# Kernel tuning notes

Measured on AMD Instinct MI355X. Metric: run time of the kernel, lower is better.

## Reference

```python
import jax, jax.numpy as jnp
import numpy as np

N = 50000      # nodes
E = 100000     # edges
F_NODE = 128
F_EDGE = 16
H = 64         # hidden_dim
OUT = 32
STEPS = 3
G = 64         # num_graphs (static; batch.max()+1 in torch)


def setup_inputs() -> dict:
    key = jax.random.key(0)
    ks = jax.random.split(key, 20)

    def lin(k, fin, fout):
        s = 1.0 / np.sqrt(fin)
        return jax.random.uniform(k, (fin, fout), jnp.float32, -s, s)

    def bias(k, fin, fout):
        s = 1.0 / np.sqrt(fin)
        return jax.random.uniform(k, (fout,), jnp.float32, -s, s)

    inp = {
        'x': jax.random.normal(ks[0], (N, F_NODE), jnp.float32),
        'edge_index': jax.random.randint(ks[1], (2, E), 0, N),
        'edge_attr': jax.random.normal(ks[2], (E, F_EDGE), jnp.float32),
        'batch': jnp.sort(jax.random.randint(ks[3], (N,), 0, G)),
        # node encoder
        'W_enc': lin(ks[4], F_NODE, H), 'b_enc': bias(ks[5], F_NODE, H),
        # edge_nn: Linear(F_EDGE,H) -> ReLU -> Linear(H, H*H)
        'W_e1': lin(ks[6], F_EDGE, H), 'b_e1': bias(ks[7], F_EDGE, H),
        'W_e2': lin(ks[8], H, H * H), 'b_e2': bias(ks[9], H, H * H),
        # GRUCell (torch layout: [3H, H])
        'W_ih': jax.random.uniform(ks[10], (3 * H, H), jnp.float32, -1/np.sqrt(H), 1/np.sqrt(H)),
        'W_hh': jax.random.uniform(ks[11], (3 * H, H), jnp.float32, -1/np.sqrt(H), 1/np.sqrt(H)),
        'b_ih': jax.random.uniform(ks[12], (3 * H,), jnp.float32, -1/np.sqrt(H), 1/np.sqrt(H)),
        'b_hh': jax.random.uniform(ks[13], (3 * H,), jnp.float32, -1/np.sqrt(H), 1/np.sqrt(H)),
        # readout MLP: Linear(H,H) -> ReLU -> Linear(H,OUT)
        'W_r1': lin(ks[14], H, H), 'b_r1': bias(ks[15], H, H),
        'W_r2': lin(ks[16], H, OUT), 'b_r2': bias(ks[17], H, OUT),
    }
    return inp


def gru_cell(m, h, W_ih, W_hh, b_ih, b_hh):
    gi = m @ W_ih.T + b_ih   # [N, 3H]
    gh = h @ W_hh.T + b_hh
    i_r, i_z, i_n = jnp.split(gi, 3, axis=-1)
    h_r, h_z, h_n = jnp.split(gh, 3, axis=-1)
    r = jax.nn.sigmoid(i_r + h_r)
    z = jax.nn.sigmoid(i_z + h_z)
    n = jnp.tanh(i_n + r * h_n)
    return (1.0 - z) * n + z * h


def reference(x, edge_index, edge_attr, batch, W_enc, b_enc, W_e1, b_e1,
              W_e2, b_e2, W_ih, W_hh, b_ih, b_hh, W_r1, b_r1, W_r2, b_r2):
    h = x @ W_enc + b_enc                                   # [N, H]
    src, dst = edge_index[0], edge_index[1]
    # edge-conditioned weight matrices (loop-invariant; compute once)
    ew = (jax.nn.relu(edge_attr @ W_e1 + b_e1) @ W_e2 + b_e2).reshape(E, H, H)
    for _ in range(STEPS):
        msg = jnp.einsum('eij,ej->ei', ew, h[src])          # per-edge matvec
        m_agg = jax.ops.segment_sum(msg, dst, num_segments=N)
        h = gru_cell(m_agg, h, W_ih, W_hh, b_ih, b_hh)
    g = jax.ops.segment_sum(h, batch, num_segments=G)       # sum readout
    return jax.nn.relu(g @ W_r1 + b_r1) @ W_r2 + b_r2
```

## Files before the change

kernel.cpp:

```cpp
#include <hip/hip_runtime.h>
#include <hip/hip_bf16.h>
#include <math.h>

#define NN 50000
#define NE 100000
#define FN 128
#define FE 16
#define HD 64
#define OUTD 32
#define NG 64
#define ZK 65

typedef unsigned int uint;
typedef unsigned short ushort;
typedef __attribute__((ext_vector_type(8))) short short8;
typedef __attribute__((ext_vector_type(16))) float f32x16;

static __device__ __forceinline__ float bfbits2f(uint u) {
    return __builtin_bit_cast(float, u << 16);
}
static __device__ __forceinline__ uint packbf(float f0, float f1) {
    return __builtin_amdgcn_perm(__builtin_bit_cast(uint, f1),
                                 __builtin_bit_cast(uint, f0), 0x07060302u);
}
static __device__ __forceinline__ ushort f2bf(float f) {
    uint u = __builtin_bit_cast(uint, f);
    u = (u + 0x7FFFu + ((u >> 16) & 1u)) >> 16;
    return (ushort)u;
}
static __device__ __forceinline__ uint pack2rne(float f0, float f1) {
    return (uint)f2bf(f0) | ((uint)f2bf(f1) << 16);
}
static __device__ __forceinline__ float fsigmoid(float x) {
    return 1.f / (1.f + __expf(-x));
}
static __device__ __forceinline__ float ftanh(float x) {
    float t = __expf(2.f * x);
    return 1.f - 2.f / (t + 1.f);
}

#define PREP_S0 (ZK * 4096)
#define PREP_S1 (256 * 128)
__global__ void k_prep(const float* __restrict__ W_e2, const float* __restrict__ b_e2,
                       const float* __restrict__ W_ih, const float* __restrict__ W_hh,
                       ushort* __restrict__ Wtb, ushort* __restrict__ Bg) {
    int idx = blockIdx.x * 256 + threadIdx.x;
    if (idx < PREP_S0) {
        int k0 = idx >> 12, r = idx & 4095;
        int i = r >> 6, j = r & 63;
        float v = (k0 < 64) ? W_e2[k0 * 4096 + i * 64 + j] : b_e2[i * 64 + j];
        Wtb[idx] = f2bf(v);
        return;
    }
    idx -= PREP_S0;
    if (idx < PREP_S1) {
        int n = idx >> 7, k = idx & 127;
        int g = n >> 6, i = n & 63;
        float v = 0.f;
        if (g == 0)      v = (k < 64) ? W_ih[i * 64 + k]         : W_hh[i * 64 + (k - 64)];
        else if (g == 1) v = (k < 64) ? W_ih[(64 + i) * 64 + k]  : W_hh[(64 + i) * 64 + (k - 64)];
        else if (g == 2) v = (k < 64) ? W_ih[(128 + i) * 64 + k] : 0.f;
        else             v = (k < 64) ? 0.f                      : W_hh[(128 + i) * 64 + (k - 64)];
        Bg[idx] = f2bf(v);
    }
}

#define NBENC ((NN + 127) / 128)
#define NBEDG ((NE + 255) / 256)
__global__ __launch_bounds__(256, 2)
void k_enc_edge(const float* __restrict__ x, const float* __restrict__ W_enc,
                const float* __restrict__ b_enc,
                const float* __restrict__ ea, const float* __restrict__ W_e1,
                const float* __restrict__ b_e1,
                float* __restrict__ h, ushort* __restrict__ hb,
                ushort* __restrict__ zbT) {
    int t = threadIdx.x;
    if (blockIdx.x < NBENC) {
        __shared__ __align__(16) ushort blds[64 * 128];
        int wave = t >> 6, lane = t & 63, l31 = lane & 31, lhi = lane >> 5;
        for (int idx = t; idx < 1024; idx += 256) {
            int n = idx >> 4, p = idx & 15;
            int ssrc = p ^ (n & 15);
            int kk = ssrc * 8;
            uint4 u;
            u.x = pack2rne(W_enc[(kk + 0) * 64 + n], W_enc[(kk + 1) * 64 + n]);
            u.y = pack2rne(W_enc[(kk + 2) * 64 + n], W_enc[(kk + 3) * 64 + n]);
            u.z = pack2rne(W_enc[(kk + 4) * 64 + n], W_enc[(kk + 5) * 64 + n]);
            u.w = pack2rne(W_enc[(kk + 6) * 64 + n], W_enc[(kk + 7) * 64 + n]);
            *(uint4*)&blds[idx * 8] = u;
        }
        int node0 = blockIdx.x * 128 + wave * 32;
        int m = node0 + l31;
        int mc = (m < NN) ? m : NN - 1;
        short8 afr[8];
        const float* xr = x + (size_t)mc * 128;
        #pragma unroll
        for (int ks = 0; ks < 8; ks++) {
            float4 v0 = *(const float4*)(xr + ks * 16 + lhi * 8);
            float4 v1 = *(const float4*)(xr + ks * 16 + lhi * 8 + 4);
            uint4 u;
            u.x = pack2rne(v0.x, v0.y); u.y = pack2rne(v0.z, v0.w);
            u.z = pack2rne(v1.x, v1.y); u.w = pack2rne(v1.z, v1.w);
            afr[ks] = __builtin_bit_cast(short8, u);
        }
        __syncthreads();
        #pragma unroll
        for (int ct = 0; ct < 2; ct++) {
            f32x16 acc = {0};
            int n = ct * 32 + l31;
            #pragma unroll
            for (int ks = 0; ks < 8; ks++) {
                int sp = (ks * 2 + lhi) ^ (n & 15);
                short8 bf = *(const short8*)&blds[n * 128 + sp * 8];
                acc = __builtin_amdgcn_mfma_f32_32x32x16_bf16(afr[ks], bf, acc, 0, 0, 0);
            }
            int o = ct * 32 + l31;
            float bias = b_enc[o];
            #pragma unroll
            for (int r = 0; r < 16; r++) {
                int row = (r & 3) + 8 * (r >> 2) + 4 * lhi;
                int node = node0 + row;
                if (node < NN) {
                    float v = acc[r] + bias;
                    h[node * 64 + o] = v;
                    hb[node * 64 + o] = f2bf(v);
                }
            }
        }
    } else {
        __shared__ float Ws[16 * 64];
        __shared__ float b1s[64];
        for (int idx = t; idx < 1024; idx += 256) Ws[idx] = W_e1[idx];
        if (t < 64) b1s[t] = b_e1[t];
        __syncthreads();
        int e = (blockIdx.x - NBENC) * 256 + t;
        int ec = (e < NE) ? e : NE - 1;
        float eav[16];
        const float4* ep = (const float4*)(ea + ec * 16);
        #pragma unroll
        for (int q = 0; q < 4; q++) {
            float4 v = ep[q];
            eav[q * 4 + 0] = v.x; eav[q * 4 + 1] = v.y; eav[q * 4 + 2] = v.z; eav[q * 4 + 3] = v.w;
        }
        if (e >= NE) return;
        #pragma unroll 4
        for (int k = 0; k < 64; k++) {
            float acc = b1s[k];
            #pragma unroll
            for (int f = 0; f < 16; f++) acc += eav[f] * Ws[f * 64 + k];
            zbT[(size_t)k * NE + e] = f2bf(fmaxf(acc, 0.f));
        }
        zbT[(size_t)64 * NE + e] = f2bf(1.0f);
    }
}

__global__ __launch_bounds__(256, 2)
void k_message(const ushort* __restrict__ zbT, const ushort* __restrict__ hb,
               const int* __restrict__ eidx, const ushort* __restrict__ Wtb,
               float* __restrict__ m_agg) {
    __shared__ __align__(16) ushort wlds[2][2 * 4096];
    __shared__ __align__(16) ushort zlds[72 * 256];
    __shared__ int sdst[256];

    int t = threadIdx.x;
    int wave = t >> 6, lane = t & 63;
    int l31 = lane & 31, lhi = lane >> 5;
    int eblk = blockIdx.x * 256;
    int e0 = eblk + wave * 64;

    {
        int e = eblk + t; if (e >= NE) e = NE - 1;
        sdst[t] = eidx[NE + e];
    }

    float hf[2][32];
    #pragma unroll
    for (int mt = 0; mt < 2; mt++) {
        int e = e0 + mt * 32 + l31;
        int ec = (e < NE) ? e : NE - 1;
        int s = eidx[ec];
        const ushort* hrow = hb + (size_t)s * 64;
        #pragma unroll
        for (int c = 0; c < 4; c++) {
            uint4 v = *(const uint4*)(hrow + c * 16 + lhi * 8);
            hf[mt][c * 8 + 0] = bfbits2f(v.x & 0xFFFFu); hf[mt][c * 8 + 1] = bfbits2f(v.x >> 16);
            hf[mt][c * 8 + 2] = bfbits2f(v.y & 0xFFFFu); hf[mt][c * 8 + 3] = bfbits2f(v.y >> 16);
            hf[mt][c * 8 + 4] = bfbits2f(v.z & 0xFFFFu); hf[mt][c * 8 + 5] = bfbits2f(v.z >> 16);
            hf[mt][c * 8 + 6] = bfbits2f(v.w & 0xFFFFu); hf[mt][c * 8 + 7] = bfbits2f(v.w >> 16);
        }
    }

    #pragma unroll
    for (int call = 0; call < 9; call++) {
        int slot = call * 256 + t;
        int k0 = slot >> 5; if (k0 > 64) k0 = 64;
        int p = slot & 31;
        const ushort* src = zbT + (size_t)k0 * NE + eblk + p * 8;
        __builtin_amdgcn_global_load_lds(
            (const __attribute__((address_space(1))) void*)src,
            (__attribute__((address_space(3))) void*)&zlds[(size_t)(call * 256 + wave * 64) * 8],
            16, 0, 0);
    }

    auto stagew = [&](int slab0, int buf) {
        #pragma unroll
        for (int call = 0; call < 4; call++) {
            int slot = call * 256 + t;
            int slab = slab0 + (slot >> 9);
            if (slab > 64) slab = 64;
            int w = slot & 511;
            int i = w >> 3, jbp = w & 7;
            int jbg = jbp ^ (i & 7);
            const ushort* src = Wtb + (size_t)slab * 4096 + i * 64 + jbg * 8;
            __builtin_amdgcn_global_load_lds(
                (const __attribute__((address_space(1))) void*)src,
                (__attribute__((address_space(3))) void*)&wlds[buf][(size_t)(call * 256 + wave * 64) * 8],
                16, 0, 0);
        }
    };
    stagew(0, 0);

    f32x16 acc00 = {0}, acc01 = {0}, acc10 = {0}, acc11 = {0};

    for (int rnd = 0; rnd < 33; rnd++) {
        __syncthreads();
        int buf = rnd & 1;
        if (rnd < 32) stagew(2 * rnd + 2, buf ^ 1);
        int nk = (rnd < 32) ? 2 : 1;
        #pragma unroll 2
        for (int kk = 0; kk < nk; kk++) {
            int k0 = 2 * rnd + kk;
            float zf0 = bfbits2f((uint)zlds[k0 * 256 + wave * 64 + l31]);
            float zf1 = bfbits2f((uint)zlds[k0 * 256 + wave * 64 + 32 + l31]);
            const ushort* wb = &wlds[buf][kk * 4096];
            #pragma unroll
            for (int c = 0; c < 4; c++) {
                int jb = c * 2 + lhi;
                short8 b0 = *(const short8*)&wb[((0 * 32 + l31) << 6) + ((jb ^ (l31 & 7)) << 3)];
                short8 b1 = *(const short8*)&wb[((32 + l31) << 6) + ((jb ^ (l31 & 7)) << 3)];
                uint4 au0, au1;
                au0.x = packbf(zf0 * hf[0][c * 8 + 0], zf0 * hf[0][c * 8 + 1]);
                au0.y = packbf(zf0 * hf[0][c * 8 + 2], zf0 * hf[0][c * 8 + 3]);
                au0.z = packbf(zf0 * hf[0][c * 8 + 4], zf0 * hf[0][c * 8 + 5]);
                au0.w = packbf(zf0 * hf[0][c * 8 + 6], zf0 * hf[0][c * 8 + 7]);
                au1.x = packbf(zf1 * hf[1][c * 8 + 0], zf1 * hf[1][c * 8 + 1]);
                au1.y = packbf(zf1 * hf[1][c * 8 + 2], zf1 * hf[1][c * 8 + 3]);
                au1.z = packbf(zf1 * hf[1][c * 8 + 4], zf1 * hf[1][c * 8 + 5]);
                au1.w = packbf(zf1 * hf[1][c * 8 + 6], zf1 * hf[1][c * 8 + 7]);
                short8 a0 = __builtin_bit_cast(short8, au0);
                short8 a1 = __builtin_bit_cast(short8, au1);
                acc00 = __builtin_amdgcn_mfma_f32_32x32x16_bf16(a0, b0, acc00, 0, 0, 0);
                acc01 = __builtin_amdgcn_mfma_f32_32x32x16_bf16(a0, b1, acc01, 0, 0, 0);
                acc10 = __builtin_amdgcn_mfma_f32_32x32x16_bf16(a1, b0, acc10, 0, 0, 0);
                acc11 = __builtin_amdgcn_mfma_f32_32x32x16_bf16(a1, b1, acc11, 0, 0, 0);
            }
        }
    }

    #pragma unroll
    for (int r = 0; r < 16; r++) {
        int roff = (r & 3) + 8 * (r >> 2) + 4 * lhi;
        int eA = e0 + roff, eB = e0 + 32 + roff;
        if (eA < NE) {
            int d0 = sdst[wave * 64 + roff];
            atomicAdd(m_agg + d0 * 64 + l31,      acc00[r]);
            atomicAdd(m_agg + d0 * 64 + 32 + l31, acc01[r]);
        }
        if (eB < NE) {
            int d1 = sdst[wave * 64 + 32 + roff];
            atomicAdd(m_agg + d1 * 64 + l31,      acc10[r]);
            atomicAdd(m_agg + d1 * 64 + 32 + l31, acc11[r]);
        }
    }
}

__global__ __launch_bounds__(256, 2)
void k_gru(const float* __restrict__ magg, const float* __restrict__ h,
           const ushort* __restrict__ hb, const ushort* __restrict__ Bg,
           const float* __restrict__ b_ih, const float* __restrict__ b_hh,
           float* __restrict__ h_out, ushort* __restrict__ hb_out) {
    __shared__ __align__(16) ushort blds[256 * 128];
    int t = threadIdx.x;
    int wave = t >> 6, lane = t & 63, l31 = lane & 31, lhi = lane >> 5;
    for (int idx = t; idx < 4096; idx += 256) {
        int n = idx >> 4, p = idx & 15;
        int ssrc = p ^ (n & 15);
        *(uint4*)&blds[idx * 8] = *(const uint4*)&Bg[n * 128 + ssrc * 8];
    }
    int node0 = blockIdx.x * 128 + wave * 32;
    int m = node0 + l31;
    int mc = (m < NN) ? m : NN - 1;
    short8 afr[8];
    const float* mrow = magg + (size_t)mc * 64;
    #pragma unroll
    for (int ks = 0; ks < 4; ks++) {
        float4 v0 = *(const float4*)(mrow + ks * 16 + lhi * 8);
        float4 v1 = *(const float4*)(mrow + ks * 16 + lhi * 8 + 4);
        uint4 u;
        u.x = pack2rne(v0.x, v0.y); u.y = pack2rne(v0.z, v0.w);
        u.z = pack2rne(v1.x, v1.y); u.w = pack2rne(v1.z, v1.w);
        afr[ks] = __builtin_bit_cast(short8, u);
    }
    const ushort* hrow = hb + (size_t)mc * 64;
    #pragma unroll
    for (int ks = 4; ks < 8; ks++) {
        uint4 v = *(const uint4*)(hrow + (ks - 4) * 16 + lhi * 8);
        afr[ks] = __builtin_bit_cast(short8, v);
    }
    __syncthreads();
    #pragma unroll
    for (int ct = 0; ct < 2; ct++) {
        f32x16 aR = {0}, aZ = {0}, aI = {0}, aH = {0};
        int nR = 0   + ct * 32 + l31;
        int nZ = 64  + ct * 32 + l31;
        int nI = 128 + ct * 32 + l31;
        int nH = 192 + ct * 32 + l31;
        #pragma unroll
        for (int ks = 0; ks < 8; ks++) {
            int s = ks * 2 + lhi;
            short8 a = afr[ks];
            short8 bR = *(const short8*)&blds[nR * 128 + (s ^ (nR & 15)) * 8];
            short8 bZ = *(const short8*)&blds[nZ * 128 + (s ^ (nZ & 15)) * 8];
            short8 bI = *(const short8*)&blds[nI * 128 + (s ^ (nI & 15)) * 8];
            short8 bH = *(const short8*)&blds[nH * 128 + (s ^ (nH & 15)) * 8];
            aR = __builtin_amdgcn_mfma_f32_32x32x16_bf16(a, bR, aR, 0, 0, 0);
            aZ = __builtin_amdgcn_mfma_f32_32x32x16_bf16(a, bZ, aZ, 0, 0, 0);
            aI = __builtin_amdgcn_mfma_f32_32x32x16_bf16(a, bI, aI, 0, 0, 0);
            aH = __builtin_amdgcn_mfma_f32_32x32x16_bf16(a, bH, aH, 0, 0, 0);
        }
        int i = ct * 32 + l31;
        float brv = b_ih[i] + b_hh[i];
        float bzv = b_ih[64 + i] + b_hh[64 + i];
        float biv = b_ih[128 + i];
        float bhv = b_hh[128 + i];
        #pragma unroll
        for (int r = 0; r < 16; r++) {
            int row = (r & 3) + 8 * (r >> 2) + 4 * lhi;
            int node = node0 + row;
            if (node < NN) {
                float ho = h[node * 64 + i];
                float rg = fsigmoid(aR[r] + brv);
                float zg = fsigmoid(aZ[r] + bzv);
                float ng = ftanh(aI[r] + biv + rg * (aH[r] + bhv));
                float hv = (1.f - zg) * ng + zg * ho;
                h_out[node * 64 + i] = hv;
                hb_out[node * 64 + i] = f2bf(hv);
            }
        }
    }
}

__global__ __launch_bounds__(256)
void k_scatter_g(const float* __restrict__ h, const int* __restrict__ batch,
                 float* __restrict__ g) {
    int t = threadIdx.x;
    int i = t & 63, sub = t >> 6;
    int n0 = blockIdx.x * 64 + sub * 16;
    if (n0 >= NN) return;
    float acc = 0.f;
    int curg = batch[n0];
    for (int q = 0; q < 16; q++) {
        int n = n0 + q;
        if (n >= NN) break;
        int gq = batch[n];
        if (gq != curg) {
            atomicAdd(&g[curg * 64 + i], acc);
            acc = 0.f; curg = gq;
        }
        acc += h[n * 64 + i];
    }
    atomicAdd(&g[curg * 64 + i], acc);
}

__global__ __launch_bounds__(1024)
void k_readout(const float* __restrict__ g, const float* __restrict__ W1, const float* __restrict__ b1,
               const float* __restrict__ W2, const float* __restrict__ b2, float* __restrict__ out) {
    __shared__ float gs[64 * 64];
    __shared__ float ts[64 * 64];
    int t = threadIdx.x;
    for (int idx = t; idx < 4096; idx += 1024) gs[idx] = g[idx];
    __syncthreads();
    for (int idx = t; idx < 4096; idx += 1024) {
        int r = idx >> 6, c = idx & 63;
        float acc = b1[c];
        #pragma unroll 8
        for (int k = 0; k < 64; k++) acc += gs[r * 64 + k] * W1[k * 64 + c];
        ts[idx] = fmaxf(acc, 0.f);
    }
    __syncthreads();
    for (int idx = t; idx < 2048; idx += 1024) {
        int r = idx >> 5, c = idx & 31;
        float acc = b2[c];
        #pragma unroll 8
        for (int k = 0; k < 64; k++) acc += ts[r * 64 + k] * W2[k * 32 + c];
        out[idx] = acc;
    }
}

extern "C" void kernel_launch(void* const* d_in, const int* in_sizes, int n_in,
                              void* d_out, int out_size, void* d_ws, size_t ws_size,
                              hipStream_t stream) {
    const float* x     = (const float*)d_in[0];
    const int*   ei    = (const int*)  d_in[1];
    const float* ea    = (const float*)d_in[2];
    const int*   batch = (const int*)  d_in[3];
    const float* W_enc = (const float*)d_in[4];
    const float* b_enc = (const float*)d_in[5];
    const float* W_e1  = (const float*)d_in[6];
    const float* b_e1  = (const float*)d_in[7];
    const float* W_e2  = (const float*)d_in[8];
    const float* b_e2  = (const float*)d_in[9];
    const float* W_ih  = (const float*)d_in[10];
    const float* W_hh  = (const float*)d_in[11];
    const float* b_ih  = (const float*)d_in[12];
    const float* b_hh  = (const float*)d_in[13];
    const float* W_r1  = (const float*)d_in[14];
    const float* b_r1  = (const float*)d_in[15];
    const float* W_r2  = (const float*)d_in[16];
    const float* b_r2  = (const float*)d_in[17];
    float* out = (float*)d_out;

    float* ws    = (float*)d_ws;
    float* h     = ws;
    float* h2    = h    + NN * 64;
    float* magg  = h2   + NN * 64;
    float* g     = magg + NN * 64;
    ushort* hb   = (ushort*)(g + NG * 64);
    ushort* hb2  = hb   + NN * 64;
    ushort* zbT  = hb2  + NN * 64;
    ushort* Wtb  = zbT  + (size_t)ZK * NE;
    ushort* Bgru = Wtb  + ZK * 4096;

    hipLaunchKernelGGL(k_prep, dim3((PREP_S0 + PREP_S1 + 255) / 256), dim3(256), 0, stream,
                       W_e2, b_e2, W_ih, W_hh, Wtb, Bgru);
    hipLaunchKernelGGL(k_enc_edge, dim3(NBENC + NBEDG), dim3(256), 0, stream,
                       x, W_enc, b_enc, ea, W_e1, b_e1, h, hb, zbT);

    float* hc = h;    float* hn = h2;
    ushort* hbc = hb; ushort* hbn = hb2;
    for (int s = 0; s < 3; s++) {
        hipMemsetAsync(magg, 0, (size_t)NN * 64 * sizeof(float), stream);
        hipLaunchKernelGGL(k_message, dim3((NE + 255) / 256), dim3(256), 0, stream,
                           zbT, hbc, ei, Wtb, magg);
        hipLaunchKernelGGL(k_gru,     dim3((NN + 127) / 128), dim3(256), 0, stream,
                           magg, hc, hbc, Bgru, b_ih, b_hh, hn, hbn);
        float* tf = hc; hc = hn; hn = tf;
        ushort* tb = hbc; hbc = hbn; hbn = tb;
    }

    hipMemsetAsync(g, 0, (size_t)NG * 64 * sizeof(float), stream);
    hipLaunchKernelGGL(k_scatter_g, dim3((NN + 63) / 64), dim3(256), 0, stream, hc, batch, g);
    hipLaunchKernelGGL(k_readout,   dim3(1), dim3(1024), 0, stream, g, W_r1, b_r1, W_r2, b_r2, out);
}
```

Baseline: 444.5 us.

## Retile message kernel to 128-edge blocks and fold magg zeroing into kernels

The message kernel now works on 128 edges per block. Its four waves split the work two ways, by edge half and by output-column half. Each round stages one 64x64 weight slab instead of two, and the bias row is handled by a constant z=1 in the last round. Less LDS per block allows launch bounds of 4 blocks per SM. The per-step hipMemsetAsync of m_agg is removed: the encoder and the GRU kernel zero it inline after reading. This trades duplicated A-fragment packing across waves and more sync rounds for higher occupancy and fewer launches.

```diff
diff --git a/kernel.cpp b/kernel.cpp
--- a/kernel.cpp
+++ b/kernel.cpp
@@ -10,11 +10,13 @@
 #define OUTD 32
 #define NG 64
 #define ZK 65
+#define EB 128
 
 typedef unsigned int uint;
 typedef unsigned short ushort;
 typedef __attribute__((ext_vector_type(8))) short short8;
 typedef __attribute__((ext_vector_type(16))) float f32x16;
+typedef __attribute__((ext_vector_type(2))) float fx2;
 
 static __device__ __forceinline__ float bfbits2f(uint u) {
     return __builtin_bit_cast(float, u << 16);
@@ -73,7 +75,7 @@
                 const float* __restrict__ ea, const float* __restrict__ W_e1,
                 const float* __restrict__ b_e1,
                 float* __restrict__ h, ushort* __restrict__ hb,
-                ushort* __restrict__ zbT) {
+                ushort* __restrict__ zbT, float* __restrict__ magg) {
     int t = threadIdx.x;
     if (blockIdx.x < NBENC) {
         __shared__ __align__(16) ushort blds[64 * 128];
@@ -124,6 +126,7 @@
                     float v = acc[r] + bias;
                     h[node * 64 + o] = v;
                     hb[node * 64 + o] = f2bf(v);
+                    magg[node * 64 + o] = 0.f;
                 }
             }
         }
@@ -150,30 +153,30 @@
             for (int f = 0; f < 16; f++) acc += eav[f] * Ws[f * 64 + k];
             zbT[(size_t)k * NE + e] = f2bf(fmaxf(acc, 0.f));
         }
-        zbT[(size_t)64 * NE + e] = f2bf(1.0f);
-    }
-}
-
-__global__ __launch_bounds__(256, 2)
+    }
+}
+
+__global__ __launch_bounds__(256, 4)
 void k_message(const ushort* __restrict__ zbT, const ushort* __restrict__ hb,
                const int* __restrict__ eidx, const ushort* __restrict__ Wtb,
                float* __restrict__ m_agg) {
-    __shared__ __align__(16) ushort wlds[2][2 * 4096];
-    __shared__ __align__(16) ushort zlds[72 * 256];
-    __shared__ int sdst[256];
+    __shared__ __align__(16) ushort wlds[2][64 * 64];
+    __shared__ __align__(16) ushort zlds[64 * 128];
+    __shared__ int sdst[EB];
 
     int t = threadIdx.x;
     int wave = t >> 6, lane = t & 63;
     int l31 = lane & 31, lhi = lane >> 5;
-    int eblk = blockIdx.x * 256;
-    int e0 = eblk + wave * 64;
-
-    {
+    int eh = wave >> 1, ih = wave & 1;
+    int eblk = blockIdx.x * EB;
+    int e0 = eblk + eh * 64;
+
+    if (t < EB) {
         int e = eblk + t; if (e >= NE) e = NE - 1;
         sdst[t] = eidx[NE + e];
     }
 
-    float hf[2][32];
+    fx2 hf2[2][16];
     #pragma unroll
     for (int mt = 0; mt < 2; mt++) {
         int e = e0 + mt * 32 + l31;
@@ -183,18 +186,17 @@
         #pragma unroll
         for (int c = 0; c < 4; c++) {
             uint4 v = *(const uint4*)(hrow + c * 16 + lhi * 8);
-            hf[mt][c * 8 + 0] = bfbits2f(v.x & 0xFFFFu); hf[mt][c * 8 + 1] = bfbits2f(v.x >> 16);
-            hf[mt][c * 8 + 2] = bfbits2f(v.y & 0xFFFFu); hf[mt][c * 8 + 3] = bfbits2f(v.y >> 16);
-            hf[mt][c * 8 + 4] = bfbits2f(v.z & 0xFFFFu); hf[mt][c * 8 + 5] = bfbits2f(v.z >> 16);
-            hf[mt][c * 8 + 6] = bfbits2f(v.w & 0xFFFFu); hf[mt][c * 8 + 7] = bfbits2f(v.w >> 16);
-        }
-    }
-
-    #pragma unroll
-    for (int call = 0; call < 9; call++) {
+            hf2[mt][c * 4 + 0].x = bfbits2f(v.x & 0xFFFFu); hf2[mt][c * 4 + 0].y = bfbits2f(v.x >> 16);
+            hf2[mt][c * 4 + 1].x = bfbits2f(v.y & 0xFFFFu); hf2[mt][c * 4 + 1].y = bfbits2f(v.y >> 16);
+            hf2[mt][c * 4 + 2].x = bfbits2f(v.z & 0xFFFFu); hf2[mt][c * 4 + 2].y = bfbits2f(v.z >> 16);
+            hf2[mt][c * 4 + 3].x = bfbits2f(v.w & 0xFFFFu); hf2[mt][c * 4 + 3].y = bfbits2f(v.w >> 16);
+        }
+    }
+
+    #pragma unroll
+    for (int call = 0; call < 4; call++) {
         int slot = call * 256 + t;
-        int k0 = slot >> 5; if (k0 > 64) k0 = 64;
-        int p = slot & 31;
+        int k0 = slot >> 4, p = slot & 15;
         const ushort* src = zbT + (size_t)k0 * NE + eblk + p * 8;
         __builtin_amdgcn_global_load_lds(
             (const __attribute__((address_space(1))) void*)src,
@@ -202,14 +204,11 @@
             16, 0, 0);
     }
 
-    auto stagew = [&](int slab0, int buf) {
-        #pragma unroll
-        for (int call = 0; call < 4; call++) {
+    auto stagew = [&](int slab, int buf) {
+        #pragma unroll
+        for (int call = 0; call < 2; call++) {
             int slot = call * 256 + t;
-            int slab = slab0 + (slot >> 9);
-            if (slab > 64) slab = 64;
-            int w = slot & 511;
-            int i = w >> 3, jbp = w & 7;
+            int i = slot >> 3, jbp = slot & 7;
             int jbg = jbp ^ (i & 7);
             const ushort* src = Wtb + (size_t)slab * 4096 + i * 64 + jbg * 8;
             __builtin_amdgcn_global_load_lds(
@@ -220,65 +219,64 @@
     };
     stagew(0, 0);
 
-    f32x16 acc00 = {0}, acc01 = {0}, acc10 = {0}, acc11 = {0};
-
-    for (int rnd = 0; rnd < 33; rnd++) {
+    f32x16 acc0 = {0}, acc1 = {0};
+    const int zoff = eh * 64 + l31;
+    const int rbase = (ih * 32 + l31) * 64;
+
+    for (int rnd = 0; rnd < 65; rnd++) {
         __syncthreads();
         int buf = rnd & 1;
-        if (rnd < 32) stagew(2 * rnd + 2, buf ^ 1);
-        int nk = (rnd < 32) ? 2 : 1;
-        #pragma unroll 2
-        for (int kk = 0; kk < nk; kk++) {
-            int k0 = 2 * rnd + kk;
-            float zf0 = bfbits2f((uint)zlds[k0 * 256 + wave * 64 + l31]);
-            float zf1 = bfbits2f((uint)zlds[k0 * 256 + wave * 64 + 32 + l31]);
-            const ushort* wb = &wlds[buf][kk * 4096];
-            #pragma unroll
-            for (int c = 0; c < 4; c++) {
-                int jb = c * 2 + lhi;
-                short8 b0 = *(const short8*)&wb[((0 * 32 + l31) << 6) + ((jb ^ (l31 & 7)) << 3)];
-                short8 b1 = *(const short8*)&wb[((32 + l31) << 6) + ((jb ^ (l31 & 7)) << 3)];
-                uint4 au0, au1;
-                au0.x = packbf(zf0 * hf[0][c * 8 + 0], zf0 * hf[0][c * 8 + 1]);
-                au0.y = packbf(zf0 * hf[0][c * 8 + 2], zf0 * hf[0][c * 8 + 3]);
-                au0.z = packbf(zf0 * hf[0][c * 8 + 4], zf0 * hf[0][c * 8 + 5]);
-                au0.w = packbf(zf0 * hf[0][c * 8 + 6], zf0 * hf[0][c * 8 + 7]);
-                au1.x = packbf(zf1 * hf[1][c * 8 + 0], zf1 * hf[1][c * 8 + 1]);
-                au1.y = packbf(zf1 * hf[1][c * 8 + 2], zf1 * hf[1][c * 8 + 3]);
-                au1.z = packbf(zf1 * hf[1][c * 8 + 4], zf1 * hf[1][c * 8 + 5]);
-                au1.w = packbf(zf1 * hf[1][c * 8 + 6], zf1 * hf[1][c * 8 + 7]);
-                short8 a0 = __builtin_bit_cast(short8, au0);
-                short8 a1 = __builtin_bit_cast(short8, au1);
-                acc00 = __builtin_amdgcn_mfma_f32_32x32x16_bf16(a0, b0, acc00, 0, 0, 0);
-                acc01 = __builtin_amdgcn_mfma_f32_32x32x16_bf16(a0, b1, acc01, 0, 0, 0);
-                acc10 = __builtin_amdgcn_mfma_f32_32x32x16_bf16(a1, b0, acc10, 0, 0, 0);
-                acc11 = __builtin_amdgcn_mfma_f32_32x32x16_bf16(a1, b1, acc11, 0, 0, 0);
-            }
-        }
-    }
-
+        if (rnd < 64) stagew(rnd + 1, buf ^ 1);
+        fx2 z0, z1;
+        if (rnd < 64) {
+            float za = bfbits2f((uint)zlds[rnd * 128 + zoff]);
+            float zb = bfbits2f((uint)zlds[rnd * 128 + 32 + zoff]);
+            z0.x = za; z0.y = za; z1.x = zb; z1.y = zb;
+        } else {
+            z0.x = 1.f; z0.y = 1.f; z1 = z0;
+        }
+        const ushort* wb = wlds[buf];
+        #pragma unroll
+        for (int c = 0; c < 4; c++) {
+            int jb = c * 2 + lhi;
+            short8 bfr = *(const short8*)&wb[rbase + ((jb ^ (l31 & 7)) << 3)];
+            fx2 p0 = z0 * hf2[0][c * 4 + 0], p1 = z0 * hf2[0][c * 4 + 1];
+            fx2 p2 = z0 * hf2[0][c * 4 + 2], p3 = z0 * hf2[0][c * 4 + 3];
+            fx2 q0 = z1 * hf2[1][c * 4 + 0], q1 = z1 * hf2[1][c * 4 + 1];
+            fx2 q2 = z1 * hf2[1][c * 4 + 2], q3 = z1 * hf2[1][c * 4 + 3];
+            uint4 au0, au1;
+            au0.x = packbf(p0.x, p0.y); au0.y = packbf(p1.x, p1.y);
+            au0.z = packbf(p2.x, p2.y); au0.w = packbf(p3.x, p3.y);
+            au1.x = packbf(q0.x, q0.y); au1.y = packbf(q1.x, q1.y);
+            au1.z = packbf(q2.x, q2.y); au1.w = packbf(q3.x, q3.y);
+            short8 a0 = __builtin_bit_cast(short8, au0);
+            short8 a1 = __builtin_bit_cast(short8, au1);
+            acc0 = __builtin_amdgcn_mfma_f32_32x32x16_bf16(a0, bfr, acc0, 0, 0, 0);
+            acc1 = __builtin_amdgcn_mfma_f32_32x32x16_bf16(a1, bfr, acc1, 0, 0, 0);
+        }
+    }
+
+    int colb = ih * 32 + l31;
     #pragma unroll
     for (int r = 0; r < 16; r++) {
         int roff = (r & 3) + 8 * (r >> 2) + 4 * lhi;
         int eA = e0 + roff, eB = e0 + 32 + roff;
         if (eA < NE) {
-            int d0 = sdst[wave * 64 + roff];
-            atomicAdd(m_agg + d0 * 64 + l31,      acc00[r]);
-            atomicAdd(m_agg + d0 * 64 + 32 + l31, acc01[r]);
+            int d0 = sdst[eh * 64 + roff];
+            atomicAdd(m_agg + (size_t)d0 * 64 + colb, acc0[r]);
         }
         if (eB < NE) {
-            int d1 = sdst[wave * 64 + 32 + roff];
-            atomicAdd(m_agg + d1 * 64 + l31,      acc10[r]);
-            atomicAdd(m_agg + d1 * 64 + 32 + l31, acc11[r]);
+            int d1 = sdst[eh * 64 + 32 + roff];
+            atomicAdd(m_agg + (size_t)d1 * 64 + colb, acc1[r]);
         }
     }
 }
 
 __global__ __launch_bounds__(256, 2)
-void k_gru(const float* __restrict__ magg, const float* __restrict__ h,
+void k_gru(float* __restrict__ magg, const float* __restrict__ h,
            const ushort* __restrict__ hb, const ushort* __restrict__ Bg,
            const float* __restrict__ b_ih, const float* __restrict__ b_hh,
-           float* __restrict__ h_out, ushort* __restrict__ hb_out) {
+           float* __restrict__ h_out, ushort* __restrict__ hb_out, int zero_m) {
     __shared__ __align__(16) ushort blds[256 * 128];
     int t = threadIdx.x;
     int wave = t >> 6, lane = t & 63, l31 = lane & 31, lhi = lane >> 5;
@@ -308,6 +306,15 @@
         afr[ks] = __builtin_bit_cast(short8, v);
     }
     __syncthreads();
+    if (zero_m) {
+        float4 zz = {0.f, 0.f, 0.f, 0.f};
+        float* mw = magg + (size_t)mc * 64;
+        #pragma unroll
+        for (int ks = 0; ks < 4; ks++) {
+            *(float4*)(mw + ks * 16 + lhi * 8) = zz;
+            *(float4*)(mw + ks * 16 + lhi * 8 + 4) = zz;
+        }
+    }
     #pragma unroll
     for (int ct = 0; ct < 2; ct++) {
         f32x16 aR = {0}, aZ = {0}, aI = {0}, aH = {0};
@@ -434,16 +441,15 @@
     hipLaunchKernelGGL(k_prep, dim3((PREP_S0 + PREP_S1 + 255) / 256), dim3(256), 0, stream,
                        W_e2, b_e2, W_ih, W_hh, Wtb, Bgru);
     hipLaunchKernelGGL(k_enc_edge, dim3(NBENC + NBEDG), dim3(256), 0, stream,
-                       x, W_enc, b_enc, ea, W_e1, b_e1, h, hb, zbT);
+                       x, W_enc, b_enc, ea, W_e1, b_e1, h, hb, zbT, magg);
 
     float* hc = h;    float* hn = h2;
     ushort* hbc = hb; ushort* hbn = hb2;
     for (int s = 0; s < 3; s++) {
-        hipMemsetAsync(magg, 0, (size_t)NN * 64 * sizeof(float), stream);
-        hipLaunchKernelGGL(k_message, dim3((NE + 255) / 256), dim3(256), 0, stream,
+        hipLaunchKernelGGL(k_message, dim3((NE + EB - 1) / EB), dim3(256), 0, stream,
                            zbT, hbc, ei, Wtb, magg);
         hipLaunchKernelGGL(k_gru,     dim3((NN + 127) / 128), dim3(256), 0, stream,
-                           magg, hc, hbc, Bgru, b_ih, b_hh, hn, hbn);
+                           magg, hc, hbc, Bgru, b_ih, b_hh, hn, hbn, (s < 2) ? 1 : 0);
         float* tf = hc; hc = hn; hn = tf;
         ushort* tb = hbc; hbc = hbn; hbn = tb;
     }
```

New measurement: 488.0 us. 9.8% more time.

## Switch bf16 to fp16 MFMA, packed half multiplies, fuse magg zeroing into kernels

Applied to the files above, without the earlier changes.

Changes all low-precision storage and MFMA calls from bf16 to fp16. The message A-operand is now built with packed half multiplies rather than float multiplies plus bf16 packing. The constant-one bias row is replaced by a register constant, and W_enc is pre-transposed to fp16 in the prep kernel. The encoder and GRU weight staging now use direct global-to-LDS loads. The per-step memsets of the aggregation buffer are removed: the encoder and the GRU kernel zero it instead. This trims launches and conversion ALU work, but fp16 has a narrower range than bf16, so products could overflow or lose accuracy.

```diff
diff --git a/kernel.cpp b/kernel.cpp
--- a/kernel.cpp
+++ b/kernel.cpp
@@ -1,5 +1,5 @@
 #include <hip/hip_runtime.h>
-#include <hip/hip_bf16.h>
+#include <hip/hip_fp16.h>
 #include <math.h>
 
 #define NN 50000
@@ -10,26 +10,31 @@
 #define OUTD 32
 #define NG 64
 #define ZK 65
+#define EB 256
 
 typedef unsigned int uint;
 typedef unsigned short ushort;
 typedef __attribute__((ext_vector_type(8))) short short8;
+typedef __attribute__((ext_vector_type(8))) _Float16 half8;
+typedef __attribute__((ext_vector_type(2))) _Float16 half2v;
 typedef __attribute__((ext_vector_type(16))) float f32x16;
 
-static __device__ __forceinline__ float bfbits2f(uint u) {
-    return __builtin_bit_cast(float, u << 16);
-}
-static __device__ __forceinline__ uint packbf(float f0, float f1) {
-    return __builtin_amdgcn_perm(__builtin_bit_cast(uint, f1),
-                                 __builtin_bit_cast(uint, f0), 0x07060302u);
-}
-static __device__ __forceinline__ ushort f2bf(float f) {
-    uint u = __builtin_bit_cast(uint, f);
-    u = (u + 0x7FFFu + ((u >> 16) & 1u)) >> 16;
-    return (ushort)u;
-}
-static __device__ __forceinline__ uint pack2rne(float f0, float f1) {
-    return (uint)f2bf(f0) | ((uint)f2bf(f1) << 16);
+static __device__ __forceinline__ ushort f2h(float f) {
+    _Float16 h = (_Float16)f;
+    return __builtin_bit_cast(ushort, h);
+}
+static __device__ __forceinline__ uint pkh2(float a, float b) {
+    auto r = __builtin_amdgcn_cvt_pkrtz(a, b);
+    return __builtin_bit_cast(uint, r);
+}
+static __device__ __forceinline__ uint hmul2u(uint a, uint b) {
+    half2v x = __builtin_bit_cast(half2v, a);
+    half2v y = __builtin_bit_cast(half2v, b);
+    half2v r = x * y;
+    return __builtin_bit_cast(uint, r);
+}
+static __device__ __forceinline__ half8 u4h8(uint4 u) {
+    return __builtin_bit_cast(half8, u);
 }
 static __device__ __forceinline__ float fsigmoid(float x) {
     return 1.f / (1.f + __expf(-x));
@@ -41,15 +46,18 @@
 
 #define PREP_S0 (ZK * 4096)
 #define PREP_S1 (256 * 128)
+#define PREP_S2 (64 * 128)
 __global__ void k_prep(const float* __restrict__ W_e2, const float* __restrict__ b_e2,
                        const float* __restrict__ W_ih, const float* __restrict__ W_hh,
-                       ushort* __restrict__ Wtb, ushort* __restrict__ Bg) {
+                       const float* __restrict__ W_enc,
+                       ushort* __restrict__ Wtb, ushort* __restrict__ Bg,
+                       ushort* __restrict__ Wet) {
     int idx = blockIdx.x * 256 + threadIdx.x;
     if (idx < PREP_S0) {
         int k0 = idx >> 12, r = idx & 4095;
         int i = r >> 6, j = r & 63;
         float v = (k0 < 64) ? W_e2[k0 * 4096 + i * 64 + j] : b_e2[i * 64 + j];
-        Wtb[idx] = f2bf(v);
+        Wtb[idx] = f2h(v);
         return;
     }
     idx -= PREP_S0;
@@ -61,47 +69,53 @@
         else if (g == 1) v = (k < 64) ? W_ih[(64 + i) * 64 + k]  : W_hh[(64 + i) * 64 + (k - 64)];
         else if (g == 2) v = (k < 64) ? W_ih[(128 + i) * 64 + k] : 0.f;
         else             v = (k < 64) ? 0.f                      : W_hh[(128 + i) * 64 + (k - 64)];
-        Bg[idx] = f2bf(v);
+        Bg[idx] = f2h(v);
+        return;
+    }
+    idx -= PREP_S1;
+    if (idx < PREP_S2) {
+        int n = idx >> 7, k = idx & 127;
+        Wet[idx] = f2h(W_enc[k * 64 + n]);
     }
 }
 
 #define NBENC ((NN + 127) / 128)
 #define NBEDG ((NE + 255) / 256)
 __global__ __launch_bounds__(256, 2)
-void k_enc_edge(const float* __restrict__ x, const float* __restrict__ W_enc,
+void k_enc_edge(const float* __restrict__ x, const ushort* __restrict__ Wet,
                 const float* __restrict__ b_enc,
                 const float* __restrict__ ea, const float* __restrict__ W_e1,
                 const float* __restrict__ b_e1,
                 float* __restrict__ h, ushort* __restrict__ hb,
-                ushort* __restrict__ zbT) {
+                ushort* __restrict__ zbT, float* __restrict__ magg) {
     int t = threadIdx.x;
     if (blockIdx.x < NBENC) {
         __shared__ __align__(16) ushort blds[64 * 128];
         int wave = t >> 6, lane = t & 63, l31 = lane & 31, lhi = lane >> 5;
-        for (int idx = t; idx < 1024; idx += 256) {
-            int n = idx >> 4, p = idx & 15;
+        #pragma unroll
+        for (int call = 0; call < 4; call++) {
+            int slot = call * 256 + t;
+            int n = slot >> 4, p = slot & 15;
             int ssrc = p ^ (n & 15);
-            int kk = ssrc * 8;
-            uint4 u;
-            u.x = pack2rne(W_enc[(kk + 0) * 64 + n], W_enc[(kk + 1) * 64 + n]);
-            u.y = pack2rne(W_enc[(kk + 2) * 64 + n], W_enc[(kk + 3) * 64 + n]);
-            u.z = pack2rne(W_enc[(kk + 4) * 64 + n], W_enc[(kk + 5) * 64 + n]);
-            u.w = pack2rne(W_enc[(kk + 6) * 64 + n], W_enc[(kk + 7) * 64 + n]);
-            *(uint4*)&blds[idx * 8] = u;
+            const ushort* src = Wet + n * 128 + ssrc * 8;
+            __builtin_amdgcn_global_load_lds(
+                (const __attribute__((address_space(1))) void*)src,
+                (__attribute__((address_space(3))) void*)&blds[(size_t)slot * 8],
+                16, 0, 0);
         }
         int node0 = blockIdx.x * 128 + wave * 32;
         int m = node0 + l31;
         int mc = (m < NN) ? m : NN - 1;
-        short8 afr[8];
+        uint4 afr[8];
         const float* xr = x + (size_t)mc * 128;
         #pragma unroll
         for (int ks = 0; ks < 8; ks++) {
             float4 v0 = *(const float4*)(xr + ks * 16 + lhi * 8);
             float4 v1 = *(const float4*)(xr + ks * 16 + lhi * 8 + 4);
             uint4 u;
-            u.x = pack2rne(v0.x, v0.y); u.y = pack2rne(v0.z, v0.w);
-            u.z = pack2rne(v1.x, v1.y); u.w = pack2rne(v1.z, v1.w);
-            afr[ks] = __builtin_bit_cast(short8, u);
+            u.x = pkh2(v0.x, v0.y); u.y = pkh2(v0.z, v0.w);
+            u.z = pkh2(v1.x, v1.y); u.w = pkh2(v1.z, v1.w);
+            afr[ks] = u;
         }
         __syncthreads();
         #pragma unroll
@@ -112,7 +126,8 @@
             for (int ks = 0; ks < 8; ks++) {
                 int sp = (ks * 2 + lhi) ^ (n & 15);
                 short8 bf = *(const short8*)&blds[n * 128 + sp * 8];
-                acc = __builtin_amdgcn_mfma_f32_32x32x16_bf16(afr[ks], bf, acc, 0, 0, 0);
+                acc = __builtin_amdgcn_mfma_f32_32x32x16_f16(
+                    u4h8(afr[ks]), __builtin_bit_cast(half8, bf), acc, 0, 0, 0);
             }
             int o = ct * 32 + l31;
             float bias = b_enc[o];
@@ -123,7 +138,8 @@
                 if (node < NN) {
                     float v = acc[r] + bias;
                     h[node * 64 + o] = v;
-                    hb[node * 64 + o] = f2bf(v);
+                    hb[node * 64 + o] = f2h(v);
+                    magg[node * 64 + o] = 0.f;
                 }
             }
         }
@@ -148,9 +164,8 @@
             float acc = b1s[k];
             #pragma unroll
             for (int f = 0; f < 16; f++) acc += eav[f] * Ws[f * 64 + k];
-            zbT[(size_t)k * NE + e] = f2bf(fmaxf(acc, 0.f));
-        }
-        zbT[(size_t)64 * NE + e] = f2bf(1.0f);
+            zbT[(size_t)k * NE + e] = f2h(fmaxf(acc, 0.f));
+        }
     }
 }
 
@@ -159,13 +174,13 @@
                const int* __restrict__ eidx, const ushort* __restrict__ Wtb,
                float* __restrict__ m_agg) {
     __shared__ __align__(16) ushort wlds[2][2 * 4096];
-    __shared__ __align__(16) ushort zlds[72 * 256];
+    __shared__ __align__(16) ushort zlds[64 * 256];
     __shared__ int sdst[256];
 
     int t = threadIdx.x;
     int wave = t >> 6, lane = t & 63;
     int l31 = lane & 31, lhi = lane >> 5;
-    int eblk = blockIdx.x * 256;
+    int eblk = blockIdx.x * EB;
     int e0 = eblk + wave * 64;
 
     {
@@ -173,7 +188,7 @@
         sdst[t] = eidx[NE + e];
     }
 
-    float hf[2][32];
+    uint hw[2][16];
     #pragma unroll
     for (int mt = 0; mt < 2; mt++) {
         int e = e0 + mt * 32 + l31;
@@ -183,22 +198,19 @@
         #pragma unroll
         for (int c = 0; c < 4; c++) {
             uint4 v = *(const uint4*)(hrow + c * 16 + lhi * 8);
-            hf[mt][c * 8 + 0] = bfbits2f(v.x & 0xFFFFu); hf[mt][c * 8 + 1] = bfbits2f(v.x >> 16);
-            hf[mt][c * 8 + 2] = bfbits2f(v.y & 0xFFFFu); hf[mt][c * 8 + 3] = bfbits2f(v.y >> 16);
-            hf[mt][c * 8 + 4] = bfbits2f(v.z & 0xFFFFu); hf[mt][c * 8 + 5] = bfbits2f(v.z >> 16);
-            hf[mt][c * 8 + 6] = bfbits2f(v.w & 0xFFFFu); hf[mt][c * 8 + 7] = bfbits2f(v.w >> 16);
-        }
-    }
-
-    #pragma unroll
-    for (int call = 0; call < 9; call++) {
+            hw[mt][c * 4 + 0] = v.x; hw[mt][c * 4 + 1] = v.y;
+            hw[mt][c * 4 + 2] = v.z; hw[mt][c * 4 + 3] = v.w;
+        }
+    }
+
+    #pragma unroll
+    for (int call = 0; call < 8; call++) {
         int slot = call * 256 + t;
-        int k0 = slot >> 5; if (k0 > 64) k0 = 64;
-        int p = slot & 31;
+        int k0 = slot >> 5, p = slot & 31;
         const ushort* src = zbT + (size_t)k0 * NE + eblk + p * 8;
         __builtin_amdgcn_global_load_lds(
             (const __attribute__((address_space(1))) void*)src,
-            (__attribute__((address_space(3))) void*)&zlds[(size_t)(call * 256 + wave * 64) * 8],
+            (__attribute__((address_space(3))) void*)&zlds[(size_t)slot * 8],
             16, 0, 0);
     }
 
@@ -214,7 +226,7 @@
             const ushort* src = Wtb + (size_t)slab * 4096 + i * 64 + jbg * 8;
             __builtin_amdgcn_global_load_lds(
                 (const __attribute__((address_space(1))) void*)src,
-                (__attribute__((address_space(3))) void*)&wlds[buf][(size_t)(call * 256 + wave * 64) * 8],
+                (__attribute__((address_space(3))) void*)&wlds[buf][(size_t)(call * 256 + t) * 8],
                 16, 0, 0);
         }
     };
@@ -227,32 +239,35 @@
         int buf = rnd & 1;
         if (rnd < 32) stagew(2 * rnd + 2, buf ^ 1);
         int nk = (rnd < 32) ? 2 : 1;
-        #pragma unroll 2
         for (int kk = 0; kk < nk; kk++) {
             int k0 = 2 * rnd + kk;
-            float zf0 = bfbits2f((uint)zlds[k0 * 256 + wave * 64 + l31]);
-            float zf1 = bfbits2f((uint)zlds[k0 * 256 + wave * 64 + 32 + l31]);
+            uint zz0, zz1;
+            if (k0 < 64) {
+                uint za = zlds[k0 * 256 + wave * 64 + l31];
+                uint zb = zlds[k0 * 256 + wave * 64 + 32 + l31];
+                zz0 = za | (za << 16);
+                zz1 = zb | (zb << 16);
+            } else {
+                zz0 = 0x3C003C00u; zz1 = 0x3C003C00u;
+            }
             const ushort* wb = &wlds[buf][kk * 4096];
             #pragma unroll
             for (int c = 0; c < 4; c++) {
                 int jb = c * 2 + lhi;
-                short8 b0 = *(const short8*)&wb[((0 * 32 + l31) << 6) + ((jb ^ (l31 & 7)) << 3)];
-                short8 b1 = *(const short8*)&wb[((32 + l31) << 6) + ((jb ^ (l31 & 7)) << 3)];
+                short8 b0r = *(const short8*)&wb[(l31 << 6) + ((jb ^ (l31 & 7)) << 3)];
+                short8 b1r = *(const short8*)&wb[((32 + l31) << 6) + ((jb ^ (l31 & 7)) << 3)];
                 uint4 au0, au1;
-                au0.x = packbf(zf0 * hf[0][c * 8 + 0], zf0 * hf[0][c * 8 + 1]);
-                au0.y = packbf(zf0 * hf[0][c * 8 + 2], zf0 * hf[0][c * 8 + 3]);
-                au0.z = packbf(zf0 * hf[0][c * 8 + 4], zf0 * hf[0][c * 8 + 5]);
-                au0.w = packbf(zf0 * hf[0][c * 8 + 6], zf0 * hf[0][c * 8 + 7]);
-                au1.x = packbf(zf1 * hf[1][c * 8 + 0], zf1 * hf[1][c * 8 + 1]);
-                au1.y = packbf(zf1 * hf[1][c * 8 + 2], zf1 * hf[1][c * 8 + 3]);
-                au1.z = packbf(zf1 * hf[1][c * 8 + 4], zf1 * hf[1][c * 8 + 5]);
-                au1.w = packbf(zf1 * hf[1][c * 8 + 6], zf1 * hf[1][c * 8 + 7]);
-                short8 a0 = __builtin_bit_cast(short8, au0);
-                short8 a1 = __builtin_bit_cast(short8, au1);
-                acc00 = __builtin_amdgcn_mfma_f32_32x32x16_bf16(a0, b0, acc00, 0, 0, 0);
-                acc01 = __builtin_amdgcn_mfma_f32_32x32x16_bf16(a0, b1, acc01, 0, 0, 0);
-                acc10 = __builtin_amdgcn_mfma_f32_32x32x16_bf16(a1, b0, acc10, 0, 0, 0);
-                acc11 = __builtin_amdgcn_mfma_f32_32x32x16_bf16(a1, b1, acc11, 0, 0, 0);
+                au0.x = hmul2u(zz0, hw[0][c * 4 + 0]); au0.y = hmul2u(zz0, hw[0][c * 4 + 1]);
+                au0.z = hmul2u(zz0, hw[0][c * 4 + 2]); au0.w = hmul2u(zz0, hw[0][c * 4 + 3]);
+                au1.x = hmul2u(zz1, hw[1][c * 4 + 0]); au1.y = hmul2u(zz1, hw[1][c * 4 + 1]);
+                au1.z = hmul2u(zz1, hw[1][c * 4 + 2]); au1.w = hmul2u(zz1, hw[1][c * 4 + 3]);
+                half8 a0 = u4h8(au0), a1 = u4h8(au1);
+                half8 b0 = __builtin_bit_cast(half8, b0r);
+                half8 b1 = __builtin_bit_cast(half8, b1r);
+                acc00 = __builtin_amdgcn_mfma_f32_32x32x16_f16(a0, b0, acc00, 0, 0, 0);
+                acc01 = __builtin_amdgcn_mfma_f32_32x32x16_f16(a0, b1, acc01, 0, 0, 0);
+                acc10 = __builtin_amdgcn_mfma_f32_32x32x16_f16(a1, b0, acc10, 0, 0, 0);
+                acc11 = __builtin_amdgcn_mfma_f32_32x32x16_f16(a1, b1, acc11, 0, 0, 0);
             }
         }
     }
@@ -263,51 +278,65 @@
         int eA = e0 + roff, eB = e0 + 32 + roff;
         if (eA < NE) {
             int d0 = sdst[wave * 64 + roff];
-            atomicAdd(m_agg + d0 * 64 + l31,      acc00[r]);
-            atomicAdd(m_agg + d0 * 64 + 32 + l31, acc01[r]);
+            atomicAdd(m_agg + (size_t)d0 * 64 + l31,      acc00[r]);
+            atomicAdd(m_agg + (size_t)d0 * 64 + 32 + l31, acc01[r]);
         }
         if (eB < NE) {
             int d1 = sdst[wave * 64 + 32 + roff];
-            atomicAdd(m_agg + d1 * 64 + l31,      acc10[r]);
-            atomicAdd(m_agg + d1 * 64 + 32 + l31, acc11[r]);
+            atomicAdd(m_agg + (size_t)d1 * 64 + l31,      acc10[r]);
+            atomicAdd(m_agg + (size_t)d1 * 64 + 32 + l31, acc11[r]);
         }
     }
 }
 
 __global__ __launch_bounds__(256, 2)
-void k_gru(const float* __restrict__ magg, const float* __restrict__ h,
+void k_gru(float* __restrict__ magg, const float* __restrict__ h,
            const ushort* __restrict__ hb, const ushort* __restrict__ Bg,
            const float* __restrict__ b_ih, const float* __restrict__ b_hh,
-           float* __restrict__ h_out, ushort* __restrict__ hb_out) {
+           float* __restrict__ h_out, ushort* __restrict__ hb_out, int zero_m) {
     __shared__ __align__(16) ushort blds[256 * 128];
     int t = threadIdx.x;
     int wave = t >> 6, lane = t & 63, l31 = lane & 31, lhi = lane >> 5;
-    for (int idx = t; idx < 4096; idx += 256) {
-        int n = idx >> 4, p = idx & 15;
+    #pragma unroll
+    for (int call = 0; call < 16; call++) {
+        int slot = call * 256 + t;
+        int n = slot >> 4, p = slot & 15;
         int ssrc = p ^ (n & 15);
-        *(uint4*)&blds[idx * 8] = *(const uint4*)&Bg[n * 128 + ssrc * 8];
+        const ushort* src = Bg + n * 128 + ssrc * 8;
+        __builtin_amdgcn_global_load_lds(
+            (const __attribute__((address_space(1))) void*)src,
+            (__attribute__((address_space(3))) void*)&blds[(size_t)slot * 8],
+            16, 0, 0);
     }
     int node0 = blockIdx.x * 128 + wave * 32;
     int m = node0 + l31;
     int mc = (m < NN) ? m : NN - 1;
-    short8 afr[8];
+    uint4 afr[8];
     const float* mrow = magg + (size_t)mc * 64;
     #pragma unroll
     for (int ks = 0; ks < 4; ks++) {
         float4 v0 = *(const float4*)(mrow + ks * 16 + lhi * 8);
         float4 v1 = *(const float4*)(mrow + ks * 16 + lhi * 8 + 4);
         uint4 u;
-        u.x = pack2rne(v0.x, v0.y); u.y = pack2rne(v0.z, v0.w);
-        u.z = pack2rne(v1.x, v1.y); u.w = pack2rne(v1.z, v1.w);
-        afr[ks] = __builtin_bit_cast(short8, u);
+        u.x = pkh2(v0.x, v0.y); u.y = pkh2(v0.z, v0.w);
+        u.z = pkh2(v1.x, v1.y); u.w = pkh2(v1.z, v1.w);
+        afr[ks] = u;
     }
     const ushort* hrow = hb + (size_t)mc * 64;
     #pragma unroll
     for (int ks = 4; ks < 8; ks++) {
-        uint4 v = *(const uint4*)(hrow + (ks - 4) * 16 + lhi * 8);
-        afr[ks] = __builtin_bit_cast(short8, v);
+        afr[ks] = *(const uint4*)(hrow + (ks - 4) * 16 + lhi * 8);
     }
     __syncthreads();
+    if (zero_m) {
+        float4 zz = {0.f, 0.f, 0.f, 0.f};
+        float* mw = magg + (size_t)mc * 64;
+        #pragma unroll
+        for (int ks = 0; ks < 4; ks++) {
+            *(float4*)(mw + ks * 16 + lhi * 8) = zz;
+            *(float4*)(mw + ks * 16 + lhi * 8 + 4) = zz;
+        }
+    }
     #pragma unroll
     for (int ct = 0; ct < 2; ct++) {
         f32x16 aR = {0}, aZ = {0}, aI = {0}, aH = {0};
@@ -318,15 +347,15 @@
         #pragma unroll
         for (int ks = 0; ks < 8; ks++) {
             int s = ks * 2 + lhi;
-            short8 a = afr[ks];
+            half8 a = u4h8(afr[ks]);
             short8 bR = *(const short8*)&blds[nR * 128 + (s ^ (nR & 15)) * 8];
             short8 bZ = *(const short8*)&blds[nZ * 128 + (s ^ (nZ & 15)) * 8];
             short8 bI = *(const short8*)&blds[nI * 128 + (s ^ (nI & 15)) * 8];
             short8 bH = *(const short8*)&blds[nH * 128 + (s ^ (nH & 15)) * 8];
-            aR = __builtin_amdgcn_mfma_f32_32x32x16_bf16(a, bR, aR, 0, 0, 0);
-            aZ = __builtin_amdgcn_mfma_f32_32x32x16_bf16(a, bZ, aZ, 0, 0, 0);
-            aI = __builtin_amdgcn_mfma_f32_32x32x16_bf16(a, bI, aI, 0, 0, 0);
-            aH = __builtin_amdgcn_mfma_f32_32x32x16_bf16(a, bH, aH, 0, 0, 0);
+            aR = __builtin_amdgcn_mfma_f32_32x32x16_f16(a, __builtin_bit_cast(half8, bR), aR, 0, 0, 0);
+            aZ = __builtin_amdgcn_mfma_f32_32x32x16_f16(a, __builtin_bit_cast(half8, bZ), aZ, 0, 0, 0);
+            aI = __builtin_amdgcn_mfma_f32_32x32x16_f16(a, __builtin_bit_cast(half8, bI), aI, 0, 0, 0);
+            aH = __builtin_amdgcn_mfma_f32_32x32x16_f16(a, __builtin_bit_cast(half8, bH), aH, 0, 0, 0);
         }
         int i = ct * 32 + l31;
         float brv = b_ih[i] + b_hh[i];
@@ -344,7 +373,7 @@
                 float ng = ftanh(aI[r] + biv + rg * (aH[r] + bhv));
                 float hv = (1.f - zg) * ng + zg * ho;
                 h_out[node * 64 + i] = hv;
-                hb_out[node * 64 + i] = f2bf(hv);
+                hb_out[node * 64 + i] = f2h(hv);
             }
         }
     }
@@ -430,20 +459,20 @@
     ushort* zbT  = hb2  + NN * 64;
     ushort* Wtb  = zbT  + (size_t)ZK * NE;
     ushort* Bgru = Wtb  + ZK * 4096;
-
-    hipLaunchKernelGGL(k_prep, dim3((PREP_S0 + PREP_S1 + 255) / 256), dim3(256), 0, stream,
-                       W_e2, b_e2, W_ih, W_hh, Wtb, Bgru);
+    ushort* Wet  = Bgru + 256 * 128;
+
+    hipLaunchKernelGGL(k_prep, dim3((PREP_S0 + PREP_S1 + PREP_S2 + 255) / 256), dim3(256), 0, stream,
+                       W_e2, b_e2, W_ih, W_hh, W_enc, Wtb, Bgru, Wet);
     hipLaunchKernelGGL(k_enc_edge, dim3(NBENC + NBEDG), dim3(256), 0, stream,
-                       x, W_enc, b_enc, ea, W_e1, b_e1, h, hb, zbT);
+                       x, Wet, b_enc, ea, W_e1, b_e1, h, hb, zbT, magg);
 
     float* hc = h;    float* hn = h2;
     ushort* hbc = hb; ushort* hbn = hb2;
     for (int s = 0; s < 3; s++) {
-        hipMemsetAsync(magg, 0, (size_t)NN * 64 * sizeof(float), stream);
-        hipLaunchKernelGGL(k_message, dim3((NE + 255) / 256), dim3(256), 0, stream,
+        hipLaunchKernelGGL(k_message, dim3((NE + EB - 1) / EB), dim3(256), 0, stream,
                            zbT, hbc, ei, Wtb, magg);
         hipLaunchKernelGGL(k_gru,     dim3((NN + 127) / 128), dim3(256), 0, stream,
-                           magg, hc, hbc, Bgru, b_ih, b_hh, hn, hbn);
+                           magg, hc, hbc, Bgru, b_ih, b_hh, hn, hbn, (s < 2) ? 1 : 0);
         float* tf = hc; hc = hn; hn = tf;
         ushort* tb = hbc; hbc = hbn; hbn = tb;
     }
```

Measured after the change: 409.5 us. -7.9%, faster.
